# Optimization experiments

Hardware: AMD Instinct MI355X
Metric: run time of the kernel (lower is better)

## Reference

```python
import jax, jax.numpy as jnp
import numpy as np

N_NODES = 100000
N_EDGES = 600000
N_GRAPHS = 256
HID = 128
IN_DIM = 7
POCKET_DIM = 28
BN_EPS = 1e-5


def setup_inputs() -> dict:
    key = jax.random.key(0)
    ks = jax.random.split(key, 24)
    d = {}
    d['x'] = jax.random.normal(ks[0], (N_NODES, IN_DIM), dtype=jnp.float32)
    d['edge_index'] = jax.random.randint(ks[1], (2, N_EDGES), 0, N_NODES, dtype=jnp.int32)
    d['batch'] = jnp.sort(jax.random.randint(ks[2], (N_NODES,), 0, N_GRAPHS, dtype=jnp.int32))
    d['pocket'] = jax.random.normal(ks[3], (POCKET_DIM,), dtype=jnp.float32)
    # GCN layer weights (PyG GCNConv: lin then normalized aggregation, bias after)
    def glorot(k, shape):
        lim = np.sqrt(6.0 / (shape[0] + shape[1]))
        return jax.random.uniform(k, shape, jnp.float32, -lim, lim)
    d['W0'] = glorot(ks[4], (IN_DIM, HID)); d['b0'] = jnp.zeros((HID,), jnp.float32)
    d['W1'] = glorot(ks[5], (HID, HID)); d['b1'] = jnp.zeros((HID,), jnp.float32)
    d['W2'] = glorot(ks[6], (HID, HID)); d['b2'] = jnp.zeros((HID,), jnp.float32)
    # BatchNorm (eval mode) params for 3 layers
    d['bn_gamma'] = jax.random.uniform(ks[7], (3, HID), jnp.float32, 0.5, 1.5)
    d['bn_beta'] = 0.1 * jax.random.normal(ks[8], (3, HID), dtype=jnp.float32)
    d['bn_mean'] = 0.1 * jax.random.normal(ks[9], (3, HID), dtype=jnp.float32)
    d['bn_var'] = jax.random.uniform(ks[10], (3, HID), jnp.float32, 0.5, 1.5)
    # pocket MLP: 28 -> 64 -> 64
    d['pw1'] = glorot(ks[11], (POCKET_DIM, 64)); d['pb1'] = jnp.zeros((64,), jnp.float32)
    d['pw2'] = glorot(ks[12], (64, 64)); d['pb2'] = jnp.zeros((64,), jnp.float32)
    # classifier: 192 -> 96 -> 1
    d['cw1'] = glorot(ks[13], (HID + 64, 96)); d['cb1'] = jnp.zeros((96,), jnp.float32)
    d['cw2'] = glorot(ks[14], (96, 1)); d['cb2'] = jnp.zeros((1,), jnp.float32)
    return d


def reference(x, edge_index, batch, pocket, W0, b0, W1, b1, W2, b2,
              bn_gamma, bn_beta, bn_mean, bn_var,
              pw1, pb1, pw2, pb2, cw1, cb1, cw2, cb2):
    src, dst = edge_index[0], edge_index[1]
    n = x.shape[0]
    # degree with self-loops (GCNConv default add_self_loops=True)
    deg = jax.ops.segment_sum(jnp.ones((src.shape[0],), x.dtype), dst, num_segments=n) + 1.0
    dinv = jax.lax.rsqrt(deg)                      # [N]
    norm = dinv[src] * dinv[dst]                   # [E] edge normalization
    self_norm = (dinv * dinv)[:, None]             # [N,1] self-loop norm

    h = x
    for i, (W, b) in enumerate(((W0, b0), (W1, b1), (W2, b2))):
        hl = h @ W                                  # [N,HID]
        agg = jax.ops.segment_sum(hl[src] * norm[:, None], dst, num_segments=n)
        agg = agg + hl * self_norm + b
        # BatchNorm1d in eval mode with running stats
        bn = (agg - bn_mean[i]) * (bn_gamma[i] * jax.lax.rsqrt(bn_var[i] + BN_EPS)) + bn_beta[i]
        h = jax.nn.relu(bn)                         # dropout is identity in eval

    # global mean pool over graphs
    sums = jax.ops.segment_sum(h, batch, num_segments=N_GRAPHS)          # [B,HID]
    cnts = jax.ops.segment_sum(jnp.ones((n,), h.dtype), batch, num_segments=N_GRAPHS)
    lig = sums / jnp.maximum(cnts, 1.0)[:, None]

    # pocket MLP, broadcast to batch
    p = jax.nn.relu(pocket @ pw1 + pb1) @ pw2 + pb2                      # [64]
    pe = jnp.broadcast_to(p[None, :], (N_GRAPHS, 64))

    emb = jnp.concatenate([lig, pe], axis=1)                             # [B,192]
    logits = (jax.nn.relu(emb @ cw1 + cb1) @ cw2 + cb2)[:, 0]            # [B]
    return logits
```

## Files before the change

### kernel.cpp

```cpp
#include <hip/hip_runtime.h>

#define NN 100000
#define NE 600000
#define NG 256
#define HID 128
#define BN_EPS 1e-5f

#define SCAN_TILE 1024
#define NTILES ((NN + SCAN_TILE - 1) / SCAN_TILE)
#define MM_TILES (NN / 32)

typedef __attribute__((ext_vector_type(8))) short short8;
typedef __attribute__((ext_vector_type(4))) float float4v;

__device__ __forceinline__ unsigned short f2bf_rn(float f) {
    unsigned u = __float_as_uint(f);
    unsigned r = u + 0x7FFFu + ((u >> 16) & 1u);
    return (unsigned short)(r >> 16);
}
__device__ __forceinline__ float bf2f(unsigned short h) {
    return __uint_as_float((unsigned)h << 16);
}
__device__ __forceinline__ void unpack8(uint4 u, float* f) {
    f[0] = __uint_as_float(u.x << 16); f[1] = __uint_as_float(u.x & 0xFFFF0000u);
    f[2] = __uint_as_float(u.y << 16); f[3] = __uint_as_float(u.y & 0xFFFF0000u);
    f[4] = __uint_as_float(u.z << 16); f[5] = __uint_as_float(u.z & 0xFFFF0000u);
    f[6] = __uint_as_float(u.w << 16); f[7] = __uint_as_float(u.w & 0xFFFF0000u);
}


__global__ __launch_bounds__(256) void hist_kernel(const int* __restrict__ dst, int* __restrict__ cnt) {
    int e = blockIdx.x * blockDim.x + threadIdx.x;
    if (e < NE) atomicAdd(&cnt[dst[e]], 1);
}


__global__ __launch_bounds__(256) void scan_a(const int* __restrict__ cnt, int* __restrict__ rs,
                                              int* __restrict__ tsum, float* __restrict__ dinv,
                                              int* __restrict__ dbin) {
    __shared__ int s[256];
    __shared__ int hb[64];
    int t = threadIdx.x;
    int base = blockIdx.x * SCAN_TILE;
    int idx = base + t * 4;
    int v0 = (idx + 0 < NN) ? cnt[idx + 0] : 0;
    int v1 = (idx + 1 < NN) ? cnt[idx + 1] : 0;
    int v2 = (idx + 2 < NN) ? cnt[idx + 2] : 0;
    int v3 = (idx + 3 < NN) ? cnt[idx + 3] : 0;
    if (idx + 0 < NN) dinv[idx + 0] = rsqrtf((float)v0 + 1.0f);
    if (idx + 1 < NN) dinv[idx + 1] = rsqrtf((float)v1 + 1.0f);
    if (idx + 2 < NN) dinv[idx + 2] = rsqrtf((float)v2 + 1.0f);
    if (idx + 3 < NN) dinv[idx + 3] = rsqrtf((float)v3 + 1.0f);
    int local = v0 + v1 + v2 + v3;
    s[t] = local;
    if (t < 64) hb[t] = 0;
    __syncthreads();
    if (idx + 0 < NN) atomicAdd(&hb[v0 < 63 ? v0 : 63], 1);
    if (idx + 1 < NN) atomicAdd(&hb[v1 < 63 ? v1 : 63], 1);
    if (idx + 2 < NN) atomicAdd(&hb[v2 < 63 ? v2 : 63], 1);
    if (idx + 3 < NN) atomicAdd(&hb[v3 < 63 ? v3 : 63], 1);
    for (int off = 1; off < 256; off <<= 1) {
        int x = (t >= off) ? s[t - off] : 0;
        __syncthreads();
        s[t] += x;
        __syncthreads();
    }
    int pre = s[t] - local;
    if (t == 255) tsum[blockIdx.x] = s[255];
    if (t < 64 && hb[t]) atomicAdd(&dbin[t], hb[t]);
    if (idx + 0 < NN) rs[idx + 0] = pre; pre += v0;
    if (idx + 1 < NN) rs[idx + 1] = pre; pre += v1;
    if (idx + 2 < NN) rs[idx + 2] = pre; pre += v2;
    if (idx + 3 < NN) rs[idx + 3] = pre;
}


__global__ __launch_bounds__(256) void scan_c(int* __restrict__ rs, const int* __restrict__ tsum,
                                              int* __restrict__ cursor, const int* __restrict__ dbin,
                                              int* __restrict__ dcur, int* __restrict__ perm) {
    __shared__ int s[256];
    __shared__ int pb[64];
    __shared__ int lb[64];
    int t = threadIdx.x;
    s[t] = (t < (int)blockIdx.x && t < NTILES) ? tsum[t] : 0;
    if (t < 64) { lb[t] = 0; pb[t] = dbin[t]; }
    __syncthreads();
#pragma unroll
    for (int off = 128; off >= 1; off >>= 1) {
        if (t < off) s[t] += s[t + off];
        __syncthreads();
    }
    int tile_off = s[0];
    for (int o = 1; o < 64; o <<= 1) {
        int x = (t < 64 && t >= o) ? pb[t - o] : 0;
        __syncthreads();
        if (t < 64) pb[t] += x;
        __syncthreads();
    }
    int base = blockIdx.x * SCAN_TILE;
    int deg[4], rk[4];
#pragma unroll
    for (int k = 0; k < 4; k++) {
        int idx = base + t * 4 + k;
        deg[k] = 0; rk[k] = 0;
        if (idx < NN) {
            int d = cursor[idx];
            deg[k] = (d < 63) ? d : 63;
            rk[k] = atomicAdd(&lb[deg[k]], 1);
        }
    }
    __syncthreads();
    if (t < 64) lb[t] = (pb[t] - dbin[t]) + atomicAdd(&dcur[t], lb[t]);
    __syncthreads();
#pragma unroll
    for (int k = 0; k < 4; k++) {
        int idx = base + t * 4 + k;
        if (idx < NN) {
            int v = rs[idx] + tile_off;
            rs[idx] = v;
            cursor[idx] = v;
            perm[lb[deg[k]] + rk[k]] = idx;
        }
    }
    if (blockIdx.x == 0 && t == 0) rs[NN] = NE;
}


__global__ __launch_bounds__(256) void bucket_prep_kernel(const int* __restrict__ src, const int* __restrict__ dst,
                                                          int* __restrict__ cursor, int* __restrict__ esrc,
                                                          const float* __restrict__ W1, const float* __restrict__ W2,
                                                          unsigned short* __restrict__ w1hi, unsigned short* __restrict__ w1lo,
                                                          unsigned short* __restrict__ w2hi, unsigned short* __restrict__ w2lo,
                                                          const float* __restrict__ pocket,
                                                          const float* __restrict__ pw1, const float* __restrict__ pb1,
                                                          const float* __restrict__ pw2, const float* __restrict__ pb2,
                                                          float* __restrict__ pv, int nb) {
    if ((int)blockIdx.x < nb) {
        int e = blockIdx.x * 256 + threadIdx.x;
        if (e < NE) {
            int pos = atomicAdd(&cursor[dst[e]], 1);
            esrc[pos] = src[e];
        }
    } else if ((int)blockIdx.x < nb + 64) {
        int t = (blockIdx.x - nb) * 256 + threadIdx.x;
        int k = t >> 7, n = t & 127;
        int to = n * HID + k;
        float v1 = W1[t];
        unsigned short h1 = f2bf_rn(v1);
        w1hi[to] = h1;
        w1lo[to] = f2bf_rn(v1 - bf2f(h1));
        float v2 = W2[t];
        unsigned short h2 = f2bf_rn(v2);
        w2hi[to] = h2;
        w2lo[to] = f2bf_rn(v2 - bf2f(h2));
    } else {
        __shared__ float t1[64];
        int j = threadIdx.x;
        if (j < 64) {
            float acc = pb1[j];
            for (int k = 0; k < 28; k++) acc = fmaf(pocket[k], pw1[k * 64 + j], acc);
            t1[j] = fmaxf(acc, 0.f);
        }
        __syncthreads();
        if (j < 64) {
            float acc2 = pb2[j];
            for (int k = 0; k < 64; k++) acc2 = fmaf(t1[k], pw2[k * 64 + j], acc2);
            pv[j] = acc2;
        }
    }
}


template<int N>
__device__ __forceinline__ void bitonic_net(int* a) {
#pragma unroll
    for (int k = 2; k <= N; k <<= 1) {
#pragma unroll
        for (int j = k >> 1; j > 0; j >>= 1) {
#pragma unroll
            for (int i = 0; i < N; i++) {
                int l = i ^ j;
                if (l > i) {
                    int x = a[i], y = a[l];
                    bool up = ((i & k) == 0);
                    bool sw = (x > y) == up;
                    a[i] = sw ? y : x;
                    a[l] = sw ? x : y;
                }
            }
        }
    }
}

template<int N>
__device__ __forceinline__ void sort_reg(int* __restrict__ esrc, int e0, int d) {
    int a[N];
#pragma unroll
    for (int i = 0; i < N; i++) a[i] = (i < d) ? esrc[e0 + i] : 0x7FFFFFFF;
    bitonic_net<N>(a);
#pragma unroll
    for (int i = 0; i < N; i++) if (i < d) esrc[e0 + i] = a[i];
}

__global__ __launch_bounds__(256) void sort_buckets(const int* __restrict__ rs,
                                                    int* __restrict__ esrc,
                                                    const int* __restrict__ perm) {
    int slot = blockIdx.x * 256 + threadIdx.x;
    if (slot >= NN) return;
    int n = perm[slot];
    int e0 = rs[n], e1 = rs[n + 1];
    int d = e1 - e0;
    if (d <= 1) return;
    if (d <= 8) {
        sort_reg<8>(esrc, e0, d);
    } else if (d <= 16) {
        sort_reg<16>(esrc, e0, d);
    } else if (d <= 32) {
        sort_reg<32>(esrc, e0, d);
    } else {
        for (int i = e0 + 1; i < e1; i++) {
            int key = esrc[i];
            int j = i - 1;
            while (j >= e0 && esrc[j] > key) { esrc[j + 1] = esrc[j]; j--; }
            esrc[j + 1] = key;
        }
    }
}


__global__ __launch_bounds__(256) void l0_fused(const float* __restrict__ x,
                                                const int* __restrict__ rs,
                                                const int* __restrict__ esrc,
                                                const float* __restrict__ dinv,
                                                const float* __restrict__ W,
                                                const float* __restrict__ b,
                                                const float* __restrict__ gamma,
                                                const float* __restrict__ beta,
                                                const float* __restrict__ mean,
                                                const float* __restrict__ var,
                                                unsigned short* __restrict__ ohi) {
    int c4 = threadIdx.x & 31;
    int r8 = threadIdx.x >> 5;
    float w[7][4];
#pragma unroll
    for (int k = 0; k < 7; k++)
#pragma unroll
        for (int i = 0; i < 4; i++) w[k][i] = W[k * HID + c4 * 4 + i];
    float4 bb = ((const float4*)b)[c4];
    float4 ga = ((const float4*)gamma)[c4];
    float4 be = ((const float4*)beta)[c4];
    float4 me = ((const float4*)mean)[c4];
    float4 va = ((const float4*)var)[c4];
    float4 sc;
    sc.x = ga.x * rsqrtf(va.x + BN_EPS);
    sc.y = ga.y * rsqrtf(va.y + BN_EPS);
    sc.z = ga.z * rsqrtf(va.z + BN_EPS);
    sc.w = ga.w * rsqrtf(va.w + BN_EPS);
    int m = threadIdx.x >> 3, f = threadIdx.x & 7;
    __shared__ float s[32][8];
    int n0 = blockIdx.x * 32;
    float acc = 0.f;
    int n = n0 + m;
    if (f < 7) {
        float di = dinv[n];
        acc = x[n * 7 + f] * di * di;
        int e0 = rs[n], e1 = rs[n + 1];
        int e = e0;
        for (; e + 1 < e1; e += 2) {
            int s0 = esrc[e], s1 = esrc[e + 1];
            float w0 = dinv[s0] * di, w1 = dinv[s1] * di;
            float a0 = x[s0 * 7 + f];
            float a1 = x[s1 * 7 + f];
            acc = fmaf(a0, w0, acc);
            acc = fmaf(a1, w1, acc);
        }
        if (e < e1) {
            int s0 = esrc[e];
            acc = fmaf(x[s0 * 7 + f], dinv[s0] * di, acc);
        }
    }
    s[m][f] = acc;
    __syncthreads();
#pragma unroll
    for (int g = 0; g < 4; g++) {
        int m2 = g * 8 + r8;
        float o0 = bb.x, o1 = bb.y, o2 = bb.z, o3 = bb.w;
#pragma unroll
        for (int k = 0; k < 7; k++) {
            float xv = s[m2][k];
            o0 = fmaf(xv, w[k][0], o0);
            o1 = fmaf(xv, w[k][1], o1);
            o2 = fmaf(xv, w[k][2], o2);
            o3 = fmaf(xv, w[k][3], o3);
        }
        ushort4 hi4;
        hi4.x = f2bf_rn(fmaxf(fmaf(o0 - me.x, sc.x, be.x), 0.f));
        hi4.y = f2bf_rn(fmaxf(fmaf(o1 - me.y, sc.y, be.y), 0.f));
        hi4.z = f2bf_rn(fmaxf(fmaf(o2 - me.z, sc.z, be.z), 0.f));
        hi4.w = f2bf_rn(fmaxf(fmaf(o3 - me.w, sc.w, be.w), 0.f));
        *(ushort4*)(ohi + (size_t)(n0 + m2) * HID + c4 * 4) = hi4;
    }
}


__global__ __launch_bounds__(256) void mm_mfma(const unsigned short* __restrict__ A,
                                               const unsigned short* __restrict__ Whi,
                                               const unsigned short* __restrict__ Wlo,
                                               unsigned short* __restrict__ out) {
    int wave = threadIdx.x >> 6;
    int lane = threadIdx.x & 63;
    int mrow = lane & 15;
    int quad = lane >> 4;
    int n0 = wave * 32;

    short8 bh[2][4], bl[2][4];
#pragma unroll
    for (int ct = 0; ct < 2; ct++) {
#pragma unroll
        for (int kc = 0; kc < 4; kc++) {
            size_t off = (size_t)(n0 + ct * 16 + mrow) * HID + kc * 32 + quad * 8;
            bh[ct][kc] = *(const short8*)(Whi + off);
            bl[ct][kc] = *(const short8*)(Wlo + off);
        }
    }

    int tile = blockIdx.x;
    if (tile >= MM_TILES) return;

    short8 ah[2][4];
#pragma unroll
    for (int rt = 0; rt < 2; rt++)
#pragma unroll
        for (int kc = 0; kc < 4; kc++)
            ah[rt][kc] = *(const short8*)(A + (size_t)(tile * 32 + rt * 16 + mrow) * HID + kc * 32 + quad * 8);

    for (;;) {
        int nt = tile + gridDim.x;
        bool has_next = nt < MM_TILES;
        short8 an[2][4];
        if (has_next) {
#pragma unroll
            for (int rt = 0; rt < 2; rt++)
#pragma unroll
                for (int kc = 0; kc < 4; kc++)
                    an[rt][kc] = *(const short8*)(A + (size_t)(nt * 32 + rt * 16 + mrow) * HID + kc * 32 + quad * 8);
        }

        float4v acc[2][2];
#pragma unroll
        for (int rt = 0; rt < 2; rt++)
#pragma unroll
            for (int ct = 0; ct < 2; ct++) {
                acc[rt][ct].x = 0.f; acc[rt][ct].y = 0.f;
                acc[rt][ct].z = 0.f; acc[rt][ct].w = 0.f;
            }

#pragma unroll
        for (int kc = 0; kc < 4; kc++)
#pragma unroll
            for (int rt = 0; rt < 2; rt++)
#pragma unroll
                for (int ct = 0; ct < 2; ct++) {
                    acc[rt][ct] = __builtin_amdgcn_mfma_f32_16x16x32_bf16(ah[rt][kc], bh[ct][kc], acc[rt][ct], 0, 0, 0);
                    acc[rt][ct] = __builtin_amdgcn_mfma_f32_16x16x32_bf16(ah[rt][kc], bl[ct][kc], acc[rt][ct], 0, 0, 0);
                }

        int m0 = tile * 32;
#pragma unroll
        for (int rt = 0; rt < 2; rt++)
#pragma unroll
            for (int ct = 0; ct < 2; ct++) {
                int col = n0 + ct * 16 + mrow;
#pragma unroll
                for (int r = 0; r < 4; r++) {
                    int row = m0 + rt * 16 + quad * 4 + r;
                    out[(size_t)row * HID + col] = f2bf_rn(acc[rt][ct][r]);
                }
            }

        if (!has_next) break;
#pragma unroll
        for (int rt = 0; rt < 2; rt++)
#pragma unroll
            for (int kc = 0; kc < 4; kc++) ah[rt][kc] = an[rt][kc];
        tile = nt;
    }
}


__global__ __launch_bounds__(256) void gather_bn(const unsigned short* __restrict__ hl,
                                                 const int* __restrict__ rs,
                                                 const int* __restrict__ esrc,
                                                 const float* __restrict__ dinv,
                                                 const float* __restrict__ b,
                                                 const float* __restrict__ gamma,
                                                 const float* __restrict__ beta,
                                                 const float* __restrict__ mean,
                                                 const float* __restrict__ var,
                                                 unsigned short* __restrict__ ohi) {
    int t = blockIdx.x * blockDim.x + threadIdx.x;
    int lane = t & 15;
    int n = t >> 4;
    if (n >= NN) return;
    const uint4* hlv = (const uint4*)hl;
    float di = dinv[n];
    float dsq = di * di;

    float acc[8], v[8];
    {
        uint4 sv = hlv[(size_t)n * 16 + lane];
        unpack8(sv, v);
        float4 bA = ((const float4*)b)[lane * 2];
        float4 bB = ((const float4*)b)[lane * 2 + 1];
        acc[0] = fmaf(v[0], dsq, bA.x); acc[1] = fmaf(v[1], dsq, bA.y);
        acc[2] = fmaf(v[2], dsq, bA.z); acc[3] = fmaf(v[3], dsq, bA.w);
        acc[4] = fmaf(v[4], dsq, bB.x); acc[5] = fmaf(v[5], dsq, bB.y);
        acc[6] = fmaf(v[6], dsq, bB.z); acc[7] = fmaf(v[7], dsq, bB.w);
    }

    int e0 = rs[n], e1 = rs[n + 1];
    int e = e0;
    while (e < e1) {
        int cnt = e1 - e; cnt = cnt > 4 ? 4 : cnt;
        int sidx[4];
#pragma unroll
        for (int i = 0; i < 4; i++) sidx[i] = esrc[(i < cnt) ? e + i : e];
        uint4 rows[4];
#pragma unroll
        for (int i = 0; i < 4; i++) rows[i] = hlv[(size_t)sidx[i] * 16 + lane];
        float wgt[4];
#pragma unroll
        for (int i = 0; i < 4; i++) wgt[i] = dinv[sidx[i]] * di;
#pragma unroll
        for (int i = 0; i < 4; i++) {
            if (i < cnt) {
                unpack8(rows[i], v);
#pragma unroll
                for (int j = 0; j < 8; j++) acc[j] = fmaf(v[j], wgt[i], acc[j]);
            }
        }
        e += cnt;
    }

    float4 gA = ((const float4*)gamma)[lane * 2], gB = ((const float4*)gamma)[lane * 2 + 1];
    float4 eA = ((const float4*)beta)[lane * 2],  eB = ((const float4*)beta)[lane * 2 + 1];
    float4 mA = ((const float4*)mean)[lane * 2],  mB = ((const float4*)mean)[lane * 2 + 1];
    float4 vA = ((const float4*)var)[lane * 2],   vB = ((const float4*)var)[lane * 2 + 1];
    float o[8];
    o[0] = fmaxf(fmaf(acc[0] - mA.x, gA.x * rsqrtf(vA.x + BN_EPS), eA.x), 0.f);
    o[1] = fmaxf(fmaf(acc[1] - mA.y, gA.y * rsqrtf(vA.y + BN_EPS), eA.y), 0.f);
    o[2] = fmaxf(fmaf(acc[2] - mA.z, gA.z * rsqrtf(vA.z + BN_EPS), eA.z), 0.f);
    o[3] = fmaxf(fmaf(acc[3] - mA.w, gA.w * rsqrtf(vA.w + BN_EPS), eA.w), 0.f);
    o[4] = fmaxf(fmaf(acc[4] - mB.x, gB.x * rsqrtf(vB.x + BN_EPS), eB.x), 0.f);
    o[5] = fmaxf(fmaf(acc[5] - mB.y, gB.y * rsqrtf(vB.y + BN_EPS), eB.y), 0.f);
    o[6] = fmaxf(fmaf(acc[6] - mB.z, gB.z * rsqrtf(vB.z + BN_EPS), eB.z), 0.f);
    o[7] = fmaxf(fmaf(acc[7] - mB.w, gB.w * rsqrtf(vB.w + BN_EPS), eB.w), 0.f);

    uint4 p;
    p.x = (unsigned)f2bf_rn(o[0]) | ((unsigned)f2bf_rn(o[1]) << 16);
    p.y = (unsigned)f2bf_rn(o[2]) | ((unsigned)f2bf_rn(o[3]) << 16);
    p.z = (unsigned)f2bf_rn(o[4]) | ((unsigned)f2bf_rn(o[5]) << 16);
    p.w = (unsigned)f2bf_rn(o[6]) | ((unsigned)f2bf_rn(o[7]) << 16);
    ((uint4*)ohi)[(size_t)n * 16 + lane] = p;
}


__global__ __launch_bounds__(1024) void poolcls_kernel(const unsigned short* __restrict__ h,
                                                       const int* __restrict__ batch,
                                                       const float* __restrict__ pv,
                                                       const float* __restrict__ cw1,
                                                       const float* __restrict__ cb1,
                                                       const float* __restrict__ cw2,
                                                       const float* __restrict__ cb2,
                                                       float* __restrict__ out) {
    int g = blockIdx.x;
    int lane = threadIdx.x & 31;
    int row = threadIdx.x >> 5;
    __shared__ int se[2];
    __shared__ float emb[192];
    __shared__ float hid[96];
    if (threadIdx.x < 2) {
        int target = g + threadIdx.x;
        int lo = 0, hi = NN;
        while (lo < hi) {
            int mid = (lo + hi) >> 1;
            if (batch[mid] < target) lo = mid + 1; else hi = mid;
        }
        se[threadIdx.x] = lo;
    }
    if (threadIdx.x < 64) emb[128 + threadIdx.x] = pv[threadIdx.x];
    __syncthreads();
    int start = se[0], end = se[1];
    const uint2* h2 = (const uint2*)h;
    float4 acc = make_float4(0.f, 0.f, 0.f, 0.f);
    for (int n = start + row; n < end; n += 32) {
        uint2 u = h2[(size_t)n * 32 + lane];
        acc.x += __uint_as_float(u.x << 16);
        acc.y += __uint_as_float(u.x & 0xFFFF0000u);
        acc.z += __uint_as_float(u.y << 16);
        acc.w += __uint_as_float(u.y & 0xFFFF0000u);
    }
    __shared__ float4 part[32][32];
    part[row][lane] = acc;
    __syncthreads();
#pragma unroll
    for (int off = 16; off >= 1; off >>= 1) {
        if (row < off) {
            float4 a = part[row][lane];
            float4 c = part[row + off][lane];
            a.x += c.x; a.y += c.y; a.z += c.z; a.w += c.w;
            part[row][lane] = a;
        }
        __syncthreads();
    }
    if (row == 0) {
        float inv = 1.0f / fmaxf((float)(end - start), 1.0f);
        float4 a = part[0][lane];
        a.x *= inv; a.y *= inv; a.z *= inv; a.w *= inv;
        ((float4*)emb)[lane] = a;
    }
    __syncthreads();
    int j = threadIdx.x;
    if (j < 96) {
        float a = cb1[j];
        for (int k = 0; k < 192; k++) a = fmaf(emb[k], cw1[k * 96 + j], a);
        hid[j] = fmaxf(a, 0.f) * cw2[j];
    }
    __syncthreads();
    if (j == 0) {
        float s = cb2[0];
        for (int k = 0; k < 96; k++) s += hid[k];
        out[g] = s;
    }
}

extern "C" void kernel_launch(void* const* d_in, const int* in_sizes, int n_in,
                              void* d_out, int out_size, void* d_ws, size_t ws_size,
                              hipStream_t stream) {
    const float* x        = (const float*)d_in[0];
    const int*   eidx     = (const int*)d_in[1];
    const int*   batch    = (const int*)d_in[2];
    const float* pocket   = (const float*)d_in[3];
    const float* W0 = (const float*)d_in[4];
    const float* b0 = (const float*)d_in[5];
    const float* W1 = (const float*)d_in[6];
    const float* b1 = (const float*)d_in[7];
    const float* W2 = (const float*)d_in[8];
    const float* b2 = (const float*)d_in[9];
    const float* bn_gamma = (const float*)d_in[10];
    const float* bn_beta  = (const float*)d_in[11];
    const float* bn_mean  = (const float*)d_in[12];
    const float* bn_var   = (const float*)d_in[13];
    const float* pw1 = (const float*)d_in[14]; const float* pb1 = (const float*)d_in[15];
    const float* pw2 = (const float*)d_in[16]; const float* pb2 = (const float*)d_in[17];
    const float* cw1 = (const float*)d_in[18]; const float* cb1 = (const float*)d_in[19];
    const float* cw2 = (const float*)d_in[20]; const float* cb2 = (const float*)d_in[21];
    float* out = (float*)d_out;

    float* ws   = (float*)d_ws;
    float* dinv = ws;
    int*   cnt  = (int*)(ws + NN);
    int*   rs   = cnt + NN;
    int*   tsum = rs + NN + 1;
    int*   dbin = tsum + 128;
    int*   dcur = dbin + 64;
    int*   perm = dcur + 64;
    int*   esrc = perm + NN;
    unsigned short* w1hi = (unsigned short*)(esrc + NE);
    unsigned short* w1lo = w1hi + HID * HID;
    unsigned short* w2hi = w1lo + HID * HID;
    unsigned short* w2lo = w2hi + HID * HID;
    size_t head = (size_t)NN * 2 + (NN + 1) + 128 + 64 + 64 + NN + NE + (4 * HID * HID) / 2;
    head = (head + 3) & ~(size_t)3;
    unsigned short* A = (unsigned short*)(ws + head);
    unsigned short* B = A + (size_t)NN * HID;
    float* pv   = (float*)(B + (size_t)NN * HID);

    const int* srcp = eidx;
    const int* dstp = eidx + NE;

    const int NB = (NE + 255) / 256;

    hipMemsetAsync(cnt, 0, (size_t)(NN + NN + 1 + 128 + 64 + 64) * sizeof(int), stream);
    hist_kernel<<<NB, 256, 0, stream>>>(dstp, cnt);
    scan_a<<<NTILES, 256, 0, stream>>>(cnt, rs, tsum, dinv, dbin);
    scan_c<<<NTILES, 256, 0, stream>>>(rs, tsum, cnt, dbin, dcur, perm);
    bucket_prep_kernel<<<NB + 65, 256, 0, stream>>>(srcp, dstp, cnt, esrc,
                                                    W1, W2, w1hi, w1lo, w2hi, w2lo,
                                                    pocket, pw1, pb1, pw2, pb2, pv, NB);
    sort_buckets<<<(NN + 255) / 256, 256, 0, stream>>>(rs, esrc, perm);

    l0_fused<<<MM_TILES, 256, 0, stream>>>(x, rs, esrc, dinv, W0, b0,
                                           bn_gamma + 0 * HID, bn_beta + 0 * HID,
                                           bn_mean + 0 * HID, bn_var + 0 * HID, A);

    const int MM_BLOCKS = 1024;
    const int GA_BLOCKS = (NN * 16 + 255) / 256;

    mm_mfma<<<MM_BLOCKS, 256, 0, stream>>>(A, w1hi, w1lo, B);
    gather_bn<<<GA_BLOCKS, 256, 0, stream>>>(
        B, rs, esrc, dinv, b1,
        bn_gamma + 1 * HID, bn_beta + 1 * HID, bn_mean + 1 * HID, bn_var + 1 * HID, A);
    mm_mfma<<<MM_BLOCKS, 256, 0, stream>>>(A, w2hi, w2lo, B);
    gather_bn<<<GA_BLOCKS, 256, 0, stream>>>(
        B, rs, esrc, dinv, b2,
        bn_gamma + 2 * HID, bn_beta + 2 * HID, bn_mean + 2 * HID, bn_var + 2 * HID, A);

    poolcls_kernel<<<NG, 1024, 0, stream>>>(A, batch, pv, cw1, cb1, cw2, cb2, out);
}
```

Before: 345.7 us.

## Fuse last-layer gather with graph mean-pool partial sums

The final gather/BN/ReLU layer now pools directly, writing fp32 per-block partial sums for at most two graphs per 16-node block instead of storing bf16 node features. A smaller finalize kernel sums the partials for each graph and runs the classifier. This removes the full-feature write and the re-read in the pooling kernel, and keeps the pooled values in fp32 rather than rounding through bf16. It relies on a 16-node block spanning at most two graphs, and on NN being divisible by 16.

```diff
diff --git a/kernel.cpp b/kernel.cpp
--- a/kernel.cpp
+++ b/kernel.cpp
@@ -9,6 +9,7 @@
 #define SCAN_TILE 1024
 #define NTILES ((NN + SCAN_TILE - 1) / SCAN_TILE)
 #define MM_TILES (NN / 32)
+#define GP_BLOCKS (NN / 16)
 
 typedef __attribute__((ext_vector_type(8))) short short8;
 typedef __attribute__((ext_vector_type(4))) float float4v;
@@ -388,6 +389,62 @@
 }
 
 
+__device__ __forceinline__ void node_l2_body(const uint4* __restrict__ hlv,
+                                             const int* __restrict__ rs,
+                                             const int* __restrict__ esrc,
+                                             const float* __restrict__ dinv,
+                                             int n, int lane,
+                                             float4 bA, float4 bB,
+                                             float4 gA, float4 gB,
+                                             float4 eA, float4 eB,
+                                             float4 mA, float4 mB,
+                                             float4 vA, float4 vB,
+                                             float* __restrict__ o) {
+    float di = dinv[n];
+    float dsq = di * di;
+    float acc[8], v[8];
+    {
+        uint4 sv = hlv[(size_t)n * 16 + lane];
+        unpack8(sv, v);
+        acc[0] = fmaf(v[0], dsq, bA.x); acc[1] = fmaf(v[1], dsq, bA.y);
+        acc[2] = fmaf(v[2], dsq, bA.z); acc[3] = fmaf(v[3], dsq, bA.w);
+        acc[4] = fmaf(v[4], dsq, bB.x); acc[5] = fmaf(v[5], dsq, bB.y);
+        acc[6] = fmaf(v[6], dsq, bB.z); acc[7] = fmaf(v[7], dsq, bB.w);
+    }
+    int e0 = rs[n], e1 = rs[n + 1];
+    int e = e0;
+    while (e < e1) {
+        int cnt = e1 - e; cnt = cnt > 4 ? 4 : cnt;
+        int sidx[4];
+#pragma unroll
+        for (int i = 0; i < 4; i++) sidx[i] = esrc[(i < cnt) ? e + i : e];
+        uint4 rows[4];
+#pragma unroll
+        for (int i = 0; i < 4; i++) rows[i] = hlv[(size_t)sidx[i] * 16 + lane];
+        float wgt[4];
+#pragma unroll
+        for (int i = 0; i < 4; i++) wgt[i] = dinv[sidx[i]] * di;
+#pragma unroll
+        for (int i = 0; i < 4; i++) {
+            if (i < cnt) {
+                unpack8(rows[i], v);
+#pragma unroll
+                for (int j = 0; j < 8; j++) acc[j] = fmaf(v[j], wgt[i], acc[j]);
+            }
+        }
+        e += cnt;
+    }
+    o[0] = fmaxf(fmaf(acc[0] - mA.x, gA.x * rsqrtf(vA.x + BN_EPS), eA.x), 0.f);
+    o[1] = fmaxf(fmaf(acc[1] - mA.y, gA.y * rsqrtf(vA.y + BN_EPS), eA.y), 0.f);
+    o[2] = fmaxf(fmaf(acc[2] - mA.z, gA.z * rsqrtf(vA.z + BN_EPS), eA.z), 0.f);
+    o[3] = fmaxf(fmaf(acc[3] - mA.w, gA.w * rsqrtf(vA.w + BN_EPS), eA.w), 0.f);
+    o[4] = fmaxf(fmaf(acc[4] - mB.x, gB.x * rsqrtf(vB.x + BN_EPS), eB.x), 0.f);
+    o[5] = fmaxf(fmaf(acc[5] - mB.y, gB.y * rsqrtf(vB.y + BN_EPS), eB.y), 0.f);
+    o[6] = fmaxf(fmaf(acc[6] - mB.z, gB.z * rsqrtf(vB.z + BN_EPS), eB.z), 0.f);
+    o[7] = fmaxf(fmaf(acc[7] - mB.w, gB.w * rsqrtf(vB.w + BN_EPS), eB.w), 0.f);
+}
+
+
 __global__ __launch_bounds__(256) void gather_bn(const unsigned short* __restrict__ hl,
                                                  const int* __restrict__ rs,
                                                  const int* __restrict__ esrc,
@@ -403,59 +460,13 @@
     int n = t >> 4;
     if (n >= NN) return;
     const uint4* hlv = (const uint4*)hl;
-    float di = dinv[n];
-    float dsq = di * di;
-
-    float acc[8], v[8];
-    {
-        uint4 sv = hlv[(size_t)n * 16 + lane];
-        unpack8(sv, v);
-        float4 bA = ((const float4*)b)[lane * 2];
-        float4 bB = ((const float4*)b)[lane * 2 + 1];
-        acc[0] = fmaf(v[0], dsq, bA.x); acc[1] = fmaf(v[1], dsq, bA.y);
-        acc[2] = fmaf(v[2], dsq, bA.z); acc[3] = fmaf(v[3], dsq, bA.w);
-        acc[4] = fmaf(v[4], dsq, bB.x); acc[5] = fmaf(v[5], dsq, bB.y);
-        acc[6] = fmaf(v[6], dsq, bB.z); acc[7] = fmaf(v[7], dsq, bB.w);
-    }
-
-    int e0 = rs[n], e1 = rs[n + 1];
-    int e = e0;
-    while (e < e1) {
-        int cnt = e1 - e; cnt = cnt > 4 ? 4 : cnt;
-        int sidx[4];
-#pragma unroll
-        for (int i = 0; i < 4; i++) sidx[i] = esrc[(i < cnt) ? e + i : e];
-        uint4 rows[4];
-#pragma unroll
-        for (int i = 0; i < 4; i++) rows[i] = hlv[(size_t)sidx[i] * 16 + lane];
-        float wgt[4];
-#pragma unroll
-        for (int i = 0; i < 4; i++) wgt[i] = dinv[sidx[i]] * di;
-#pragma unroll
-        for (int i = 0; i < 4; i++) {
-            if (i < cnt) {
-                unpack8(rows[i], v);
-#pragma unroll
-                for (int j = 0; j < 8; j++) acc[j] = fmaf(v[j], wgt[i], acc[j]);
-            }
-        }
-        e += cnt;
-    }
-
-    float4 gA = ((const float4*)gamma)[lane * 2], gB = ((const float4*)gamma)[lane * 2 + 1];
-    float4 eA = ((const float4*)beta)[lane * 2],  eB = ((const float4*)beta)[lane * 2 + 1];
-    float4 mA = ((const float4*)mean)[lane * 2],  mB = ((const float4*)mean)[lane * 2 + 1];
-    float4 vA = ((const float4*)var)[lane * 2],   vB = ((const float4*)var)[lane * 2 + 1];
     float o[8];
-    o[0] = fmaxf(fmaf(acc[0] - mA.x, gA.x * rsqrtf(vA.x + BN_EPS), eA.x), 0.f);
-    o[1] = fmaxf(fmaf(acc[1] - mA.y, gA.y * rsqrtf(vA.y + BN_EPS), eA.y), 0.f);
-    o[2] = fmaxf(fmaf(acc[2] - mA.z, gA.z * rsqrtf(vA.z + BN_EPS), eA.z), 0.f);
-    o[3] = fmaxf(fmaf(acc[3] - mA.w, gA.w * rsqrtf(vA.w + BN_EPS), eA.w), 0.f);
-    o[4] = fmaxf(fmaf(acc[4] - mB.x, gB.x * rsqrtf(vB.x + BN_EPS), eB.x), 0.f);
-    o[5] = fmaxf(fmaf(acc[5] - mB.y, gB.y * rsqrtf(vB.y + BN_EPS), eB.y), 0.f);
-    o[6] = fmaxf(fmaf(acc[6] - mB.z, gB.z * rsqrtf(vB.z + BN_EPS), eB.z), 0.f);
-    o[7] = fmaxf(fmaf(acc[7] - mB.w, gB.w * rsqrtf(vB.w + BN_EPS), eB.w), 0.f);
-
+    node_l2_body(hlv, rs, esrc, dinv, n, lane,
+                 ((const float4*)b)[lane * 2], ((const float4*)b)[lane * 2 + 1],
+                 ((const float4*)gamma)[lane * 2], ((const float4*)gamma)[lane * 2 + 1],
+                 ((const float4*)beta)[lane * 2], ((const float4*)beta)[lane * 2 + 1],
+                 ((const float4*)mean)[lane * 2], ((const float4*)mean)[lane * 2 + 1],
+                 ((const float4*)var)[lane * 2], ((const float4*)var)[lane * 2 + 1], o);
     uint4 p;
     p.x = (unsigned)f2bf_rn(o[0]) | ((unsigned)f2bf_rn(o[1]) << 16);
     p.y = (unsigned)f2bf_rn(o[2]) | ((unsigned)f2bf_rn(o[3]) << 16);
@@ -465,17 +476,66 @@
 }
 
 
-__global__ __launch_bounds__(1024) void poolcls_kernel(const unsigned short* __restrict__ h,
-                                                       const int* __restrict__ batch,
-                                                       const float* __restrict__ pv,
-                                                       const float* __restrict__ cw1,
-                                                       const float* __restrict__ cb1,
-                                                       const float* __restrict__ cw2,
-                                                       const float* __restrict__ cb2,
-                                                       float* __restrict__ out) {
+__global__ __launch_bounds__(256) void gather_pool(const unsigned short* __restrict__ hl,
+                                                   const int* __restrict__ rs,
+                                                   const int* __restrict__ esrc,
+                                                   const float* __restrict__ dinv,
+                                                   const int* __restrict__ batch,
+                                                   const float* __restrict__ b,
+                                                   const float* __restrict__ gamma,
+                                                   const float* __restrict__ beta,
+                                                   const float* __restrict__ mean,
+                                                   const float* __restrict__ var,
+                                                   float* __restrict__ pb,
+                                                   int* __restrict__ gid) {
+    __shared__ float tmp[16][128];
+    __shared__ int gls[16];
+    int lane = threadIdx.x & 15;
+    int nl = threadIdx.x >> 4;
+    int n = blockIdx.x * 16 + nl;
+    const uint4* hlv = (const uint4*)hl;
+    float o[8];
+    node_l2_body(hlv, rs, esrc, dinv, n, lane,
+                 ((const float4*)b)[lane * 2], ((const float4*)b)[lane * 2 + 1],
+                 ((const float4*)gamma)[lane * 2], ((const float4*)gamma)[lane * 2 + 1],
+                 ((const float4*)beta)[lane * 2], ((const float4*)beta)[lane * 2 + 1],
+                 ((const float4*)mean)[lane * 2], ((const float4*)mean)[lane * 2 + 1],
+                 ((const float4*)var)[lane * 2], ((const float4*)var)[lane * 2 + 1], o);
+#pragma unroll
+    for (int k = 0; k < 8; k++) tmp[nl][lane * 8 + k] = o[k];
+    if (lane == 0) gls[nl] = batch[n];
+    __syncthreads();
+    int j = threadIdx.x;
+    if (j < 128) {
+        int g0 = gls[0];
+        float s0 = 0.f, s1 = 0.f;
+#pragma unroll
+        for (int i = 0; i < 16; i++) {
+            float v = tmp[i][j];
+            bool second = (gls[i] != g0);
+            s0 += second ? 0.f : v;
+            s1 += second ? v : 0.f;
+        }
+        pb[(size_t)blockIdx.x * 256 + j] = s0;
+        pb[(size_t)blockIdx.x * 256 + 128 + j] = s1;
+        if (j == 0) {
+            gid[blockIdx.x * 2] = g0;
+            gid[blockIdx.x * 2 + 1] = (gls[15] != g0) ? gls[15] : -1;
+        }
+    }
+}
+
+
+__global__ __launch_bounds__(256) void finalize_cls(const float* __restrict__ pb,
+                                                    const int* __restrict__ gid,
+                                                    const int* __restrict__ batch,
+                                                    const float* __restrict__ pv,
+                                                    const float* __restrict__ cw1,
+                                                    const float* __restrict__ cb1,
+                                                    const float* __restrict__ cw2,
+                                                    const float* __restrict__ cb2,
+                                                    float* __restrict__ out) {
     int g = blockIdx.x;
-    int lane = threadIdx.x & 31;
-    int row = threadIdx.x >> 5;
     __shared__ int se[2];
     __shared__ float emb[192];
     __shared__ float hid[96];
@@ -491,36 +551,20 @@
     if (threadIdx.x < 64) emb[128 + threadIdx.x] = pv[threadIdx.x];
     __syncthreads();
     int start = se[0], end = se[1];
-    const uint2* h2 = (const uint2*)h;
-    float4 acc = make_float4(0.f, 0.f, 0.f, 0.f);
-    for (int n = start + row; n < end; n += 32) {
-        uint2 u = h2[(size_t)n * 32 + lane];
-        acc.x += __uint_as_float(u.x << 16);
-        acc.y += __uint_as_float(u.x & 0xFFFF0000u);
-        acc.z += __uint_as_float(u.y << 16);
-        acc.w += __uint_as_float(u.y & 0xFFFF0000u);
-    }
-    __shared__ float4 part[32][32];
-    part[row][lane] = acc;
-    __syncthreads();
-#pragma unroll
-    for (int off = 16; off >= 1; off >>= 1) {
-        if (row < off) {
-            float4 a = part[row][lane];
-            float4 c = part[row + off][lane];
-            a.x += c.x; a.y += c.y; a.z += c.z; a.w += c.w;
-            part[row][lane] = a;
-        }
-        __syncthreads();
-    }
-    if (row == 0) {
+    int j = threadIdx.x;
+    if (j < 128) {
+        float s = 0.f;
+        if (end > start) {
+            int bs = start >> 4, be = (end - 1) >> 4;
+            for (int bk = bs; bk <= be; bk++) {
+                if (gid[bk * 2] == g)     s += pb[(size_t)bk * 256 + j];
+                if (gid[bk * 2 + 1] == g) s += pb[(size_t)bk * 256 + 128 + j];
+            }
+        }
         float inv = 1.0f / fmaxf((float)(end - start), 1.0f);
-        float4 a = part[0][lane];
-        a.x *= inv; a.y *= inv; a.z *= inv; a.w *= inv;
-        ((float4*)emb)[lane] = a;
-    }
-    __syncthreads();
-    int j = threadIdx.x;
+        emb[j] = s * inv;
+    }
+    __syncthreads();
     if (j < 96) {
         float a = cb1[j];
         for (int k = 0; k < 192; k++) a = fmaf(emb[k], cw1[k * 96 + j], a);
@@ -575,6 +619,8 @@
     unsigned short* A = (unsigned short*)(ws + head);
     unsigned short* B = A + (size_t)NN * HID;
     float* pv   = (float*)(B + (size_t)NN * HID);
+    float* pbuf = pv + 64;
+    int*   gid  = (int*)(pbuf + (size_t)GP_BLOCKS * 256);
 
     const int* srcp = eidx;
     const int* dstp = eidx + NE;
@@ -602,9 +648,10 @@
         B, rs, esrc, dinv, b1,
         bn_gamma + 1 * HID, bn_beta + 1 * HID, bn_mean + 1 * HID, bn_var + 1 * HID, A);
     mm_mfma<<<MM_BLOCKS, 256, 0, stream>>>(A, w2hi, w2lo, B);
-    gather_bn<<<GA_BLOCKS, 256, 0, stream>>>(
-        B, rs, esrc, dinv, b2,
-        bn_gamma + 2 * HID, bn_beta + 2 * HID, bn_mean + 2 * HID, bn_var + 2 * HID, A);
-
-    poolcls_kernel<<<NG, 1024, 0, stream>>>(A, batch, pv, cw1, cb1, cw2, cb2, out);
-}
+    gather_pool<<<GP_BLOCKS, 256, 0, stream>>>(
+        B, rs, esrc, dinv, batch, b2,
+        bn_gamma + 2 * HID, bn_beta + 2 * HID, bn_mean + 2 * HID, bn_var + 2 * HID,
+        pbuf, gid);
+
+    finalize_cls<<<NG, 256, 0, stream>>>(pbuf, gid, batch, pv, cw1, cb1, cw2, cb2, out);
+}
```

Result: no change. 349.0 us (+1.0%).
